# Kernel tuning notes

Hardware: AMD Instinct MI355X
Metric: run time of the kernel (lower is better)

## Reference

```python
import jax, jax.numpy as jnp
import numpy as np

TAU = 0.6  # BGK relaxation time (>= 0.5 per __post_init__ stability check)
# D2Q9 lattice: velocities, weights, opposite-direction indices
E = np.array([[0, 0], [1, 0], [0, 1], [-1, 0], [0, -1],
              [1, 1], [-1, 1], [-1, -1], [1, -1]], dtype=np.int32)
W = np.array([4.0 / 9] + [1.0 / 9] * 4 + [1.0 / 36] * 4, dtype=np.float32)
OPP = np.array([0, 3, 4, 1, 2, 7, 8, 5, 6], dtype=np.int32)


def setup_inputs() -> dict:
    key = jax.random.key(0)
    k1, k2, k3 = jax.random.split(key, 3)
    nx, ny = 2048, 2048
    f = jax.random.uniform(k1, (nx, ny, 9), dtype=jnp.float32)  # positive populations
    rho = jnp.sum(f, axis=-1)                                    # consistent density
    u = 0.05 * jax.random.normal(k2, (nx, ny, 2), dtype=jnp.float32)  # low-Ma velocity
    obstacle_mask = jax.random.uniform(k3, (nx, ny)) < 0.01      # sparse solid cells
    return {"f": f, "rho": rho, "u": u, "obstacle_mask": obstacle_mask}


def _equilibrium(rho, u):
    # feq_i = w_i * rho * (1 + 3 e.u + 4.5 (e.u)^2 - 1.5 u.u)
    e = jnp.asarray(E, jnp.float32)
    w = jnp.asarray(W)
    eu = jnp.einsum('xyd,qd->xyq', u, e)              # [nx, ny, 9]
    usq = jnp.sum(u * u, axis=-1, keepdims=True)       # [nx, ny, 1]
    return w * rho[..., None] * (1.0 + 3.0 * eu + 4.5 * eu * eu - 1.5 * usq)


def reference(f, rho, u, obstacle_mask):
    # --- collide (BGK) ---
    feq = _equilibrium(rho, u)
    f_star = f - (f - feq) / TAU
    # --- stream: roll each direction by its lattice velocity (lattice not shifted) ---
    f_new = jnp.stack(
        [jnp.roll(f_star[..., i], shift=(int(E[i, 0]), int(E[i, 1])), axis=(0, 1))
         for i in range(9)],
        axis=-1,
    )
    # --- obstacle bounce-back: solid cells reflect post-collision populations ---
    f_bb = f_star[..., jnp.asarray(OPP)]
    f_new = jnp.where(obstacle_mask[..., None], f_bb, f_new)
    # --- lift macro fields from post-stream distributions ---
    rho_new = jnp.sum(f_new, axis=-1)
    e = jnp.asarray(E, jnp.float32)
    u_new = jnp.einsum('xyq,qd->xyd', f_new, e) / rho_new[..., None]
    # pack (f_new [..9], rho_new [..1], u_new [..2]) -> [nx, ny, 12]
    return jnp.concatenate([f_new, rho_new[..., None], u_new], axis=-1)
```

## Files before the change

kernel.cpp:

```cpp
#include <hip/hip_runtime.h>


#define NX 2048
#define NY 2048
#define WRAP 2047

typedef float floatx4 __attribute__((ext_vector_type(4)));

__global__ __launch_bounds__(256) void lbm_step_kernel(
    const float* __restrict__ f,
    const float* __restrict__ rho,
    const float* __restrict__ u,
    const int*   __restrict__ mask,
    float*       __restrict__ out)
{
    const int y = blockIdx.x * blockDim.x + threadIdx.x;
    const int x = blockIdx.y;

    const int   ex[9] = {0, 1, 0, -1, 0, 1, -1, -1, 1};
    const int   ey[9] = {0, 0, 1, 0, -1, 1, 1, -1, -1};
    const float w9[9] = {4.0f/9.0f,
                         1.0f/9.0f, 1.0f/9.0f, 1.0f/9.0f, 1.0f/9.0f,
                         1.0f/36.0f, 1.0f/36.0f, 1.0f/36.0f, 1.0f/36.0f};
    const float INV_TAU = 1.0f / 0.6f;

    const float2* __restrict__ u2 = reinterpret_cast<const float2*>(u);

    float fn[9];

    #pragma unroll
    for (int i = 0; i < 9; ++i) {
        const int xs  = (x - ex[i]) & WRAP;
        const int ys  = (y - ey[i]) & WRAP;
        const int idx = xs * NY + ys;
        const float  rn = rho[idx];
        const float2 uv = u2[idx];
        const float eu  = (float)ex[i] * uv.x + (float)ey[i] * uv.y;
        const float usq = uv.x * uv.x + uv.y * uv.y;
        const float feq = w9[i] * rn * (1.0f + 3.0f * eu + 4.5f * eu * eu - 1.5f * usq);
        const float fi  = f[idx * 9 + i];
        fn[i] = fi - (fi - feq) * INV_TAU;
    }

    const int cidx = x * NY + y;

    if (mask[cidx]) {
        const float  rn = rho[cidx];
        const float2 uv = u2[cidx];
        const float usq = uv.x * uv.x + uv.y * uv.y;
        float fs[9];
        #pragma unroll
        for (int i = 0; i < 9; ++i) {
            const float eu  = (float)ex[i] * uv.x + (float)ey[i] * uv.y;
            const float feq = w9[i] * rn * (1.0f + 3.0f * eu + 4.5f * eu * eu - 1.5f * usq);
            const float fi  = f[cidx * 9 + i];
            fs[i] = fi - (fi - feq) * INV_TAU;
        }
        const int opp[9] = {0, 3, 4, 1, 2, 7, 8, 5, 6};
        #pragma unroll
        for (int i = 0; i < 9; ++i) fn[i] = fs[opp[i]];
    }

    const float rhon = fn[0] + fn[1] + fn[2] + fn[3] + fn[4]
                     + fn[5] + fn[6] + fn[7] + fn[8];
    const float uxn = (fn[1] - fn[3] + fn[5] - fn[6] - fn[7] + fn[8]) / rhon;
    const float uyn = (fn[2] - fn[4] + fn[5] + fn[6] - fn[7] - fn[8]) / rhon;

    floatx4* o4 = reinterpret_cast<floatx4*>(out + (size_t)cidx * 12);
    floatx4 o0; o0.x = fn[0]; o0.y = fn[1]; o0.z = fn[2]; o0.w = fn[3];
    floatx4 o1; o1.x = fn[4]; o1.y = fn[5]; o1.z = fn[6]; o1.w = fn[7];
    floatx4 o2; o2.x = fn[8]; o2.y = rhon;  o2.z = uxn;   o2.w = uyn;
    __builtin_nontemporal_store(o0, o4 + 0);
    __builtin_nontemporal_store(o1, o4 + 1);
    __builtin_nontemporal_store(o2, o4 + 2);
}

extern "C" void kernel_launch(void* const* d_in, const int* in_sizes, int n_in,
                              void* d_out, int out_size, void* d_ws, size_t ws_size,
                              hipStream_t stream) {
    const float* f    = (const float*)d_in[0];
    const float* rho  = (const float*)d_in[1];
    const float* u    = (const float*)d_in[2];
    const int*   mask = (const int*)d_in[3];
    float* out = (float*)d_out;

    dim3 block(256, 1, 1);
    dim3 grid(NY / 256, NX, 1);
    lbm_step_kernel<<<grid, block, 0, stream>>>(f, rho, u, mask, out);
}
```

Before: 411.0 us.

## Stage collided halo tile in LDS and stage outputs for coalesced stores

Each block now covers a 4x64 tile. It first loads a halo of 6x66 cells, computes the collision once per population into shared memory, and then streams by reading neighbours from LDS. Before, each thread recomputed the equilibrium from rho and u at nine neighbour locations and did strided gathers of f. The outputs are also staged through LDS so they are written as contiguous float4 stores. The cost is a halo overhead of about 1.55x redundant loads per tile, two extra barriers, and integer div/mod index math. The stride-13 LDS staging may also cause bank conflicts.

Result: faster. 376.7 us (-8.3%).

```diff
diff --git a/kernel.cpp b/kernel.cpp
--- a/kernel.cpp
+++ b/kernel.cpp
@@ -4,6 +4,12 @@
 #define NX 2048
 #define NY 2048
 #define WRAP 2047
+#define TR 4
+#define TC 64
+#define HR (TR + 2)
+#define HC (TC + 2)
+#define HCELLS (HR * HC)
+#define HELEMS (HCELLS * 9)
 
 typedef float floatx4 __attribute__((ext_vector_type(4)));
 
@@ -14,51 +20,61 @@
     const int*   __restrict__ mask,
     float*       __restrict__ out)
 {
-    const int y = blockIdx.x * blockDim.x + threadIdx.x;
-    const int x = blockIdx.y;
+    __shared__ float lds[HELEMS];
 
-    const int   ex[9] = {0, 1, 0, -1, 0, 1, -1, -1, 1};
-    const int   ey[9] = {0, 0, 1, 0, -1, 1, 1, -1, -1};
-    const float w9[9] = {4.0f/9.0f,
-                         1.0f/9.0f, 1.0f/9.0f, 1.0f/9.0f, 1.0f/9.0f,
-                         1.0f/36.0f, 1.0f/36.0f, 1.0f/36.0f, 1.0f/36.0f};
+    const int tid = threadIdx.x;
+    const int y0 = blockIdx.x * TC;
+    const int x0 = blockIdx.y * TR;
     const float INV_TAU = 1.0f / 0.6f;
 
     const float2* __restrict__ u2 = reinterpret_cast<const float2*>(u);
 
+    for (int k = tid; k < HELEMS; k += 256) {
+        const unsigned cell = (unsigned)k / 9u;
+        const int i  = k - (int)cell * 9;
+        const unsigned hr = cell / (unsigned)HC;
+        const int hc = (int)cell - (int)hr * HC;
+        const int xr = (x0 - 1 + (int)hr) & WRAP;
+        const int yc = (y0 - 1 + hc) & WRAP;
+        const int g  = xr * NY + yc;
+
+        const float  rn = rho[g];
+        const float2 uv = u2[g];
+        const float  fi = f[(size_t)g * 9 + i];
+
+        const float exf = (float)((int)((0x20919u >> (2 * i)) & 3u) - 1);
+        const float eyf = (float)((int)((0x2865u  >> (2 * i)) & 3u) - 1);
+        const float wi  = (i == 0) ? (4.0f / 9.0f)
+                                   : ((i < 5) ? (1.0f / 9.0f) : (1.0f / 36.0f));
+        const float eu  = exf * uv.x + eyf * uv.y;
+        const float usq = uv.x * uv.x + uv.y * uv.y;
+        const float feq = wi * rn * (1.0f + 3.0f * eu + 4.5f * eu * eu - 1.5f * usq);
+        lds[k] = fi - (fi - feq) * INV_TAU;
+    }
+    __syncthreads();
+
+    const int r = tid >> 6;
+    const int c = tid & 63;
+    const int ex9[9]  = {0, 1, 0, -1, 0, 1, -1, -1, 1};
+    const int ey9[9]  = {0, 0, 1, 0, -1, 1, 1, -1, -1};
+    const int opp9[9] = {0, 3, 4, 1, 2, 7, 8, 5, 6};
+
     float fn[9];
-
     #pragma unroll
     for (int i = 0; i < 9; ++i) {
-        const int xs  = (x - ex[i]) & WRAP;
-        const int ys  = (y - ey[i]) & WRAP;
-        const int idx = xs * NY + ys;
-        const float  rn = rho[idx];
-        const float2 uv = u2[idx];
-        const float eu  = (float)ex[i] * uv.x + (float)ey[i] * uv.y;
-        const float usq = uv.x * uv.x + uv.y * uv.y;
-        const float feq = w9[i] * rn * (1.0f + 3.0f * eu + 4.5f * eu * eu - 1.5f * usq);
-        const float fi  = f[idx * 9 + i];
-        fn[i] = fi - (fi - feq) * INV_TAU;
+        const int lsrc = (r + 1 - ex9[i]) * HC + (c + 1 - ey9[i]);
+        fn[i] = lds[lsrc * 9 + i];
     }
 
+    const int x = x0 + r, y = y0 + c;
     const int cidx = x * NY + y;
-
     if (mask[cidx]) {
-        const float  rn = rho[cidx];
-        const float2 uv = u2[cidx];
-        const float usq = uv.x * uv.x + uv.y * uv.y;
+        const int lc = (r + 1) * HC + (c + 1);
         float fs[9];
         #pragma unroll
-        for (int i = 0; i < 9; ++i) {
-            const float eu  = (float)ex[i] * uv.x + (float)ey[i] * uv.y;
-            const float feq = w9[i] * rn * (1.0f + 3.0f * eu + 4.5f * eu * eu - 1.5f * usq);
-            const float fi  = f[cidx * 9 + i];
-            fs[i] = fi - (fi - feq) * INV_TAU;
-        }
-        const int opp[9] = {0, 3, 4, 1, 2, 7, 8, 5, 6};
+        for (int i = 0; i < 9; ++i) fs[i] = lds[lc * 9 + i];
         #pragma unroll
-        for (int i = 0; i < 9; ++i) fn[i] = fs[opp[i]];
+        for (int i = 0; i < 9; ++i) fn[i] = fs[opp9[i]];
     }
 
     const float rhon = fn[0] + fn[1] + fn[2] + fn[3] + fn[4]
@@ -66,13 +82,32 @@
     const float uxn = (fn[1] - fn[3] + fn[5] - fn[6] - fn[7] + fn[8]) / rhon;
     const float uyn = (fn[2] - fn[4] + fn[5] + fn[6] - fn[7] - fn[8]) / rhon;
 
-    floatx4* o4 = reinterpret_cast<floatx4*>(out + (size_t)cidx * 12);
-    floatx4 o0; o0.x = fn[0]; o0.y = fn[1]; o0.z = fn[2]; o0.w = fn[3];
-    floatx4 o1; o1.x = fn[4]; o1.y = fn[5]; o1.z = fn[6]; o1.w = fn[7];
-    floatx4 o2; o2.x = fn[8]; o2.y = rhon;  o2.z = uxn;   o2.w = uyn;
-    __builtin_nontemporal_store(o0, o4 + 0);
-    __builtin_nontemporal_store(o1, o4 + 1);
-    __builtin_nontemporal_store(o2, o4 + 2);
+    __syncthreads();
+
+    {
+        const int b = tid * 13;
+        #pragma unroll
+        for (int i = 0; i < 9; ++i) lds[b + i] = fn[i];
+        lds[b + 9]  = rhon;
+        lds[b + 10] = uxn;
+        lds[b + 11] = uyn;
+    }
+    __syncthreads();
+
+    for (int k4 = tid; k4 < TR * TC * 3; k4 += 256) {
+        const unsigned r2  = (unsigned)k4 / 192u;
+        const int      rem = k4 - (int)r2 * 192;
+        const unsigned cc  = (unsigned)rem / 3u;
+        const int      q   = rem - (int)cc * 3;
+        const int lbase = (int)r2 * (TC * 13) + (int)cc * 13 + q * 4;
+        floatx4 v;
+        v.x = lds[lbase + 0];
+        v.y = lds[lbase + 1];
+        v.z = lds[lbase + 2];
+        v.w = lds[lbase + 3];
+        const size_t obase = ((size_t)(x0 + (int)r2) * NY + y0) * 12 + (size_t)rem * 4;
+        __builtin_nontemporal_store(v, reinterpret_cast<floatx4*>(out + obase));
+    }
 }
 
 extern "C" void kernel_launch(void* const* d_in, const int* in_sizes, int n_in,
@@ -85,6 +120,6 @@
     float* out = (float*)d_out;
 
     dim3 block(256, 1, 1);
-    dim3 grid(NY / 256, NX, 1);
+    dim3 grid(NY / TC, NX / TR, 1);
     lbm_step_kernel<<<grid, block, 0, stream>>>(f, rho, u, mask, out);
 }
```
